# Performance work log

Measured on AMD Instinct MI355X. Metric: run time of the kernel, lower is better.

## Reference

```python
import jax, jax.numpy as jnp
import numpy as np

H = 4      # attention heads
C = 64     # hidden_dim per head
GAT_SLOPE = 0.2   # PyG GATConv leaky_relu negative_slope
ACT_SLOPE = 0.01  # nn.LeakyReLU / F.leaky_relu default


def gat_layer(x, src, dst, W, a_src, a_dst, b, n):
    # x: [n, F_in] -> h: [n, H, C]
    h = (x @ W).reshape(n, H, C)
    al_s = jnp.einsum('nhc,hc->nh', h, a_src)  # [n, H]
    al_d = jnp.einsum('nhc,hc->nh', h, a_dst)
    e = jax.nn.leaky_relu(al_s[src] + al_d[dst], GAT_SLOPE)  # [E, H]
    # segment softmax over destination nodes (self-loops ensure non-empty segments)
    m = jax.ops.segment_max(e, dst, num_segments=n)
    p = jnp.exp(e - m[dst])
    s = jax.ops.segment_sum(p, dst, num_segments=n)
    alpha = p / s[dst]
    out = jax.ops.segment_sum(h[src] * alpha[:, :, None], dst, num_segments=n)  # [n, H, C]
    return out.reshape(n, H * C) + b


def setup_inputs() -> dict:
    key = jax.random.key(0)
    ks = jax.random.split(key, 24)
    N, E = 102400, 409600
    F_IN, F_OUT = 80, 80
    HC = H * C
    RIN, RHID, ROUT = 60, 512, 60
    def g(k, shape, scale):
        return (jax.random.normal(k, shape, dtype=jnp.float32) * scale)
    inp = {
        'x': g(ks[0], (N, F_IN), 1.0),
        'edge_index': jax.random.randint(ks[1], (2, E), 0, N, dtype=jnp.int64),
        'root_ctx_norm': g(ks[2], (4096, RIN), 1.0),
        'W0': g(ks[3], (F_IN, HC), 0.1), 'a_src0': g(ks[4], (H, C), 0.1), 'a_dst0': g(ks[5], (H, C), 0.1), 'b0': jnp.zeros((HC,), jnp.float32),
        'W1': g(ks[6], (HC, HC), 0.06), 'a_src1': g(ks[7], (H, C), 0.1), 'a_dst1': g(ks[8], (H, C), 0.1), 'b1': jnp.zeros((HC,), jnp.float32),
        'W2': g(ks[9], (HC, HC), 0.06), 'a_src2': g(ks[10], (H, C), 0.1), 'a_dst2': g(ks[11], (H, C), 0.1), 'b2': jnp.zeros((HC,), jnp.float32),
        'fc_w': g(ks[12], (HC, F_OUT), 0.06), 'fc_b': jnp.zeros((F_OUT,), jnp.float32),
        'r_w1': g(ks[13], (RIN, RHID), 0.1), 'r_b1': jnp.zeros((RHID,), jnp.float32),
        'r_w2': g(ks[14], (RHID, RHID), 0.04), 'r_b2': jnp.zeros((RHID,), jnp.float32),
        'r_w3': g(ks[15], (RHID, ROUT), 0.04), 'r_b3': jnp.zeros((ROUT,), jnp.float32),
    }
    return inp


def reference(x, edge_index, root_ctx_norm,
              W0, a_src0, a_dst0, b0,
              W1, a_src1, a_dst1, b1,
              W2, a_src2, a_dst2, b2,
              fc_w, fc_b, r_w1, r_b1, r_w2, r_b2, r_w3, r_b3):
    n = x.shape[0]
    loops = jnp.arange(n, dtype=edge_index.dtype)
    src = jnp.concatenate([edge_index[0], loops])  # PyG add_self_loops=True
    dst = jnp.concatenate([edge_index[1], loops])
    h = gat_layer(x, src, dst, W0, a_src0, a_dst0, b0, n)
    h = jax.nn.leaky_relu(h, ACT_SLOPE)  # dropout is identity in eval
    h = gat_layer(h, src, dst, W1, a_src1, a_dst1, b1, n)
    h = jax.nn.leaky_relu(h, ACT_SLOPE)
    h = gat_layer(h, src, dst, W2, a_src2, a_dst2, b2, n)
    rot = h @ fc_w + fc_b
    r = jax.nn.leaky_relu(root_ctx_norm @ r_w1 + r_b1, ACT_SLOPE)
    r = jax.nn.leaky_relu(r @ r_w2 + r_b2, ACT_SLOPE)
    root_norm = r @ r_w3 + r_b3
    return rot, root_norm
```

## Files before the change

### kernel.cpp

```cpp
#include <hip/hip_runtime.h>
#include <hip/hip_bf16.h>


#define GAT_SLOPE 0.2f
#define ACT_SLOPE 0.01f

typedef unsigned short ushort_t;
typedef __attribute__((ext_vector_type(8))) short bf16x8;
typedef __attribute__((ext_vector_type(8))) unsigned short ushort8;
typedef __attribute__((ext_vector_type(4))) unsigned short ushort4v;
typedef __attribute__((ext_vector_type(4))) float floatx4;

__device__ __forceinline__ float lrelu(float x, float s) {
    return fmaxf(x, s * x);
}

__device__ __forceinline__ ushort_t f2bf(float f) {
    union { float f; unsigned u; } x; x.f = f;
    unsigned r = x.u + 0x7FFF + ((x.u >> 16) & 1);
    return (ushort_t)(r >> 16);
}

__device__ __forceinline__ float bf2f(ushort_t u) {
    union { unsigned u; float f; } x; x.u = ((unsigned)u) << 16;
    return x.f;
}

__global__ void detect_fmt(const int* __restrict__ raw, int nwords, int* flag) {
    __shared__ int nz;
    if (threadIdx.x == 0) nz = 0;
    __syncthreads();
    int lim = nwords < 4096 ? nwords : 4096;
    for (int i = threadIdx.x * 2 + 1; i < lim; i += 512)
        if (raw[i] != 0) atomicAdd(&nz, 1);
    __syncthreads();
    if (threadIdx.x == 0) *flag = (nz == 0) ? 1 : 0;
}

__global__ void zero2(int* __restrict__ a, int* __restrict__ b, int n) {
    int i = blockIdx.x * blockDim.x + threadIdx.x;
    if (i < n) { a[i] = 0; b[i] = 0; }
}

__global__ void convert_count(const int* __restrict__ raw, int E,
                              const int* __restrict__ flag,
                              int* __restrict__ idx32, int* __restrict__ counts) {
    int i = blockIdx.x * blockDim.x + threadIdx.x;
    if (i >= E) return;
    int f = *flag;
    int s = f ? raw[2 * i] : raw[i];
    int d = f ? raw[2 * (E + i)] : raw[E + i];
    idx32[i] = s;
    idx32[E + i] = d;
    atomicAdd(&counts[d], 1);
}

__global__ void scan_block(const int* __restrict__ counts, int* __restrict__ inc,
                           int* __restrict__ blockSums, int N) {
    __shared__ int sh[256];
    int i = blockIdx.x * 256 + threadIdx.x;
    int v = (i < N) ? counts[i] : 0;
    sh[threadIdx.x] = v;
    __syncthreads();
    for (int off = 1; off < 256; off <<= 1) {
        int t = (threadIdx.x >= off) ? sh[threadIdx.x - off] : 0;
        __syncthreads();
        sh[threadIdx.x] += t;
        __syncthreads();
    }
    if (i < N) inc[i] = sh[threadIdx.x];
    if (threadIdx.x == 255) blockSums[blockIdx.x] = sh[255];
}

__global__ void scan_sums(int* __restrict__ blockSums, int nb, int* __restrict__ row_ptr) {
    __shared__ int sh[512];
    int v = ((int)threadIdx.x < nb) ? blockSums[threadIdx.x] : 0;
    sh[threadIdx.x] = v;
    __syncthreads();
    for (int off = 1; off < 512; off <<= 1) {
        int t = (threadIdx.x >= off) ? sh[threadIdx.x - off] : 0;
        __syncthreads();
        sh[threadIdx.x] += t;
        __syncthreads();
    }
    if ((int)threadIdx.x < nb) blockSums[threadIdx.x] = sh[threadIdx.x];
    if (threadIdx.x == 0) row_ptr[0] = 0;
}

__global__ void scan_add(const int* __restrict__ inc, const int* __restrict__ blockSums,
                         int* __restrict__ row_ptr, int N) {
    int i = blockIdx.x * 256 + threadIdx.x;
    if (i < N) row_ptr[i + 1] = inc[i] + (blockIdx.x > 0 ? blockSums[blockIdx.x - 1] : 0);
}

__global__ void edge_fill(const int* __restrict__ src, const int* __restrict__ dst, int E,
                          const int* __restrict__ row_ptr, int* __restrict__ cursor,
                          int* __restrict__ col) {
    int i = blockIdx.x * blockDim.x + threadIdx.x;
    if (i < E) {
        int d = dst[i];
        int pos = row_ptr[d] + atomicAdd(&cursor[d], 1);
        col[pos] = src[i];
    }
}

__global__ void convert_bf4(const float* __restrict__ in, ushort_t* __restrict__ out, int n4) {
    int i = blockIdx.x * blockDim.x + threadIdx.x;
    if (i >= n4) return;
    const float4 v = ((const float4*)in)[i];
    ushort4v o;
    o.x = f2bf(v.x); o.y = f2bf(v.y); o.z = f2bf(v.z); o.w = f2bf(v.w);
    ((ushort4v*)out)[i] = o;
}

__global__ void convert_padrow(const float* __restrict__ in, ushort_t* __restrict__ out,
                               int M, int Kr, int Kp) {
    int i = blockIdx.x * blockDim.x + threadIdx.x;
    if (i >= M * Kp) return;
    int r = i / Kp, c = i - r * Kp;
    out[i] = f2bf((c < Kr) ? in[(size_t)r * Kr + c] : 0.f);
}

struct WConv { const float* in; ushort_t* out; int Kp, Kr, N, Npad, blkOff; };
struct WConvArr { WConv e[7]; int n; };

__global__ void convert_w_multi(WConvArr a) {
    int b = blockIdx.x;
    int ei = 0;
    for (int k = 1; k < a.n; k++)
        if (b >= a.e[k].blkOff) ei = k;
    WConv w = a.e[ei];
    int i = (b - w.blkOff) * 256 + threadIdx.x;
    if (i >= w.Npad * w.Kp) return;
    int n = i / w.Kp, k = i - n * w.Kp;
    float v = (n < w.N && k < w.Kr) ? w.in[(size_t)k * w.N + n] : 0.f;
    w.out[i] = f2bf(v);
}

#define LDA 40

__global__ __launch_bounds__(256) void gemm_mfma_gat(
    const ushort_t* __restrict__ A, const ushort_t* __restrict__ Bt,
    const float* __restrict__ a_src, const float* __restrict__ a_dst,
    ushort_t* __restrict__ Hbf, float* __restrict__ al_s, float* __restrict__ al_d,
    int M, int K) {
    const int NCOL = 256;
    __shared__ __align__(16) ushort_t As[128 * LDA];
    __shared__ __align__(16) ushort_t Bs[128 * LDA];
    int t = threadIdx.x;
    int wave = t >> 6, lane = t & 63;
    int wm = (wave >> 1) << 6;
    int wn = (wave & 1) << 6;
    int rowBase = blockIdx.y << 7;
    int colBase = blockIdx.x << 7;
    int lrow = lane & 15, lquad = lane >> 4;
    floatx4 acc[4][4];
#pragma unroll
    for (int i = 0; i < 4; i++)
#pragma unroll
        for (int j = 0; j < 4; j++) acc[i][j] = (floatx4){0.f, 0.f, 0.f, 0.f};

    int srow = t >> 2;
    int sko  = (t & 3) * 8;
    const ushort8 zero8 = {0, 0, 0, 0, 0, 0, 0, 0};

    for (int k0 = 0; k0 < K; k0 += 32) {
        bool kin = (k0 + sko + 8) <= K;
#pragma unroll
        for (int half = 0; half < 2; half++) {
            int row = srow + half * 64;
            ushort8 va = kin ? *(const ushort8*)(A + (size_t)(rowBase + row) * K + k0 + sko)
                             : zero8;
            *(ushort8*)(As + row * LDA + sko) = va;
            ushort8 vb = kin ? *(const ushort8*)(Bt + (size_t)(colBase + row) * K + k0 + sko)
                             : zero8;
            *(ushort8*)(Bs + row * LDA + sko) = vb;
        }
        __syncthreads();
        bf16x8 af[4], bfv[4];
#pragma unroll
        for (int i = 0; i < 4; i++)
            af[i] = *(const bf16x8*)(As + (wm + i * 16 + lrow) * LDA + lquad * 8);
#pragma unroll
        for (int j = 0; j < 4; j++)
            bfv[j] = *(const bf16x8*)(Bs + (wn + j * 16 + lrow) * LDA + lquad * 8);
#pragma unroll
        for (int i = 0; i < 4; i++)
#pragma unroll
            for (int j = 0; j < 4; j++)
                acc[i][j] = __builtin_amdgcn_mfma_f32_16x16x32_bf16(af[i], bfv[j],
                                                                    acc[i][j], 0, 0, 0);
        __syncthreads();
    }
    int head = (colBase + wn) >> 6;
    float avs[4], avd[4];
#pragma unroll
    for (int j = 0; j < 4; j++) {
        avs[j] = a_src[head * 64 + j * 16 + lrow];
        avd[j] = a_dst[head * 64 + j * 16 + lrow];
    }
#pragma unroll
    for (int i = 0; i < 4; i++) {
#pragma unroll
        for (int r = 0; r < 4; r++) {
            float ps = 0.f, pd = 0.f;
#pragma unroll
            for (int j = 0; j < 4; j++) {
                ps += acc[i][j][r] * avs[j];
                pd += acc[i][j][r] * avd[j];
            }
#pragma unroll
            for (int off = 1; off < 16; off <<= 1) {
                ps += __shfl_xor(ps, off);
                pd += __shfl_xor(pd, off);
            }
            if (lrow == 0) {
                int gr = rowBase + wm + i * 16 + lquad * 4 + r;
                al_s[gr * 4 + head] = ps;
                al_d[gr * 4 + head] = pd;
            }
        }
        int grb = rowBase + wm + i * 16 + lquad * 4;
#pragma unroll
        for (int j = 0; j < 4; j++) {
            int gc = colBase + wn + j * 16 + lrow;
#pragma unroll
            for (int r = 0; r < 4; r++)
                Hbf[(size_t)(grb + r) * NCOL + gc] = f2bf(acc[i][j][r]);
        }
    }
}

__global__ __launch_bounds__(256) void gemm_mfma(
    const ushort_t* __restrict__ A, const ushort_t* __restrict__ Bt,
    const float* __restrict__ bias, void* __restrict__ Cout,
    int M, int N, int K, int act, float slope, int outBf) {
    __shared__ __align__(16) ushort_t As[128 * LDA];
    __shared__ __align__(16) ushort_t Bs[128 * LDA];
    int t = threadIdx.x;
    int wave = t >> 6, lane = t & 63;
    int wm = (wave >> 1) << 6;
    int wn = (wave & 1) << 6;
    int rowBase = blockIdx.y << 7;
    int colBase = blockIdx.x << 7;
    int lrow = lane & 15, lquad = lane >> 4;
    floatx4 acc[4][4];
#pragma unroll
    for (int i = 0; i < 4; i++)
#pragma unroll
        for (int j = 0; j < 4; j++) acc[i][j] = (floatx4){0.f, 0.f, 0.f, 0.f};

    int srow = t >> 2;
    int sko  = (t & 3) * 8;
    const ushort8 zero8 = {0, 0, 0, 0, 0, 0, 0, 0};

    for (int k0 = 0; k0 < K; k0 += 32) {
        bool kin = (k0 + sko + 8) <= K;
#pragma unroll
        for (int half = 0; half < 2; half++) {
            int row = srow + half * 64;
            ushort8 va = kin ? *(const ushort8*)(A + (size_t)(rowBase + row) * K + k0 + sko)
                             : zero8;
            *(ushort8*)(As + row * LDA + sko) = va;
            ushort8 vb = kin ? *(const ushort8*)(Bt + (size_t)(colBase + row) * K + k0 + sko)
                             : zero8;
            *(ushort8*)(Bs + row * LDA + sko) = vb;
        }
        __syncthreads();
        bf16x8 af[4], bfv[4];
#pragma unroll
        for (int i = 0; i < 4; i++)
            af[i] = *(const bf16x8*)(As + (wm + i * 16 + lrow) * LDA + lquad * 8);
#pragma unroll
        for (int j = 0; j < 4; j++)
            bfv[j] = *(const bf16x8*)(Bs + (wn + j * 16 + lrow) * LDA + lquad * 8);
#pragma unroll
        for (int i = 0; i < 4; i++)
#pragma unroll
            for (int j = 0; j < 4; j++)
                acc[i][j] = __builtin_amdgcn_mfma_f32_16x16x32_bf16(af[i], bfv[j],
                                                                    acc[i][j], 0, 0, 0);
        __syncthreads();
    }
#pragma unroll
    for (int i = 0; i < 4; i++) {
        int gr = rowBase + wm + i * 16 + lquad * 4;
#pragma unroll
        for (int j = 0; j < 4; j++) {
            int gc = colBase + wn + j * 16 + lrow;
            if (gc >= N) continue;
            float b = bias ? bias[gc] : 0.f;
#pragma unroll
            for (int r = 0; r < 4; r++) {
                float v = acc[i][j][r] + b;
                if (act) v = lrelu(v, slope);
                if (outBf)
                    ((ushort_t*)Cout)[(size_t)(gr + r) * N + gc] = f2bf(v);
                else
                    ((float*)Cout)[(size_t)(gr + r) * N + gc] = v;
            }
        }
    }
}

__global__ __launch_bounds__(256) void gat_agg(
    const ushort_t* __restrict__ h_bf, const float* __restrict__ al_s,
    const float* __restrict__ al_d, const int* __restrict__ row_ptr,
    const int* __restrict__ col, const float* __restrict__ bias,
    ushort_t* __restrict__ out_bf, int N, int act, float slope) {
    int gw = __builtin_amdgcn_readfirstlane((blockIdx.x * 256 + threadIdx.x) >> 6);
    if (gw >= N) return;
    int lane = threadIdx.x & 63;
    int head = lane >> 4;
    int idx = gw * 4 + head;
    float ad = al_d[idx];
    const ushort4v* h4 = (const ushort4v*)h_bf;
    float p = __expf(lrelu(al_s[idx] + ad, GAT_SLOPE));
    ushort4v hv = h4[(size_t)gw * 64 + lane];
    float s = p;
    float4 acc;
    acc.x = p * bf2f(hv.x); acc.y = p * bf2f(hv.y);
    acc.z = p * bf2f(hv.z); acc.w = p * bf2f(hv.w);
    int beg = row_ptr[gw], end = row_ptr[gw + 1];
    for (int i = beg; i < end; i += 4) {
        int cnt = end - i;
        int sn0 = col[i];
        int sn1 = (cnt > 1) ? col[i + 1] : sn0;
        int sn2 = (cnt > 2) ? col[i + 2] : sn0;
        int sn3 = (cnt > 3) ? col[i + 3] : sn0;
        ushort4v h0 = h4[(size_t)sn0 * 64 + lane];
        ushort4v h1 = h4[(size_t)sn1 * 64 + lane];
        ushort4v h2 = h4[(size_t)sn2 * 64 + lane];
        ushort4v h3 = h4[(size_t)sn3 * 64 + lane];
        float a0 = al_s[sn0 * 4 + head];
        float a1 = al_s[sn1 * 4 + head];
        float a2 = al_s[sn2 * 4 + head];
        float a3 = al_s[sn3 * 4 + head];
        float p0 = __expf(lrelu(a0 + ad, GAT_SLOPE));
        acc.x += p0 * bf2f(h0.x); acc.y += p0 * bf2f(h0.y);
        acc.z += p0 * bf2f(h0.z); acc.w += p0 * bf2f(h0.w);
        s += p0;
        if (cnt > 1) {
            float p1 = __expf(lrelu(a1 + ad, GAT_SLOPE));
            acc.x += p1 * bf2f(h1.x); acc.y += p1 * bf2f(h1.y);
            acc.z += p1 * bf2f(h1.z); acc.w += p1 * bf2f(h1.w);
            s += p1;
        }
        if (cnt > 2) {
            float p2 = __expf(lrelu(a2 + ad, GAT_SLOPE));
            acc.x += p2 * bf2f(h2.x); acc.y += p2 * bf2f(h2.y);
            acc.z += p2 * bf2f(h2.z); acc.w += p2 * bf2f(h2.w);
            s += p2;
        }
        if (cnt > 3) {
            float p3 = __expf(lrelu(a3 + ad, GAT_SLOPE));
            acc.x += p3 * bf2f(h3.x); acc.y += p3 * bf2f(h3.y);
            acc.z += p3 * bf2f(h3.z); acc.w += p3 * bf2f(h3.w);
            s += p3;
        }
    }
    float rs = 1.f / s;
    float4 bv = ((const float4*)bias)[lane];
    acc.x = acc.x * rs + bv.x; acc.y = acc.y * rs + bv.y;
    acc.z = acc.z * rs + bv.z; acc.w = acc.w * rs + bv.w;
    if (act) {
        acc.x = lrelu(acc.x, slope); acc.y = lrelu(acc.y, slope);
        acc.z = lrelu(acc.z, slope); acc.w = lrelu(acc.w, slope);
    }
    ushort4v o;
    o.x = f2bf(acc.x); o.y = f2bf(acc.y); o.z = f2bf(acc.z); o.w = f2bf(acc.w);
    ((ushort4v*)out_bf)[(size_t)gw * 64 + lane] = o;
}

extern "C" void kernel_launch(void* const* d_in, const int* in_sizes, int n_in,
                              void* d_out, int out_size, void* d_ws, size_t ws_size,
                              hipStream_t stream) {
    const float* x        = (const float*)d_in[0];
    const int*   rawEdge  = (const int*)d_in[1];
    const float* rootCtx  = (const float*)d_in[2];
    const float* W[3]     = {(const float*)d_in[3], (const float*)d_in[7], (const float*)d_in[11]};
    const float* aS[3]    = {(const float*)d_in[4], (const float*)d_in[8], (const float*)d_in[12]};
    const float* aD[3]    = {(const float*)d_in[5], (const float*)d_in[9], (const float*)d_in[13]};
    const float* bb[3]    = {(const float*)d_in[6], (const float*)d_in[10], (const float*)d_in[14]};
    const float* fc_w     = (const float*)d_in[15];
    const float* fc_b     = (const float*)d_in[16];
    const float* r_w1     = (const float*)d_in[17];
    const float* r_b1     = (const float*)d_in[18];
    const float* r_w2     = (const float*)d_in[19];
    const float* r_b2     = (const float*)d_in[20];
    const float* r_w3     = (const float*)d_in[21];
    const float* r_b3     = (const float*)d_in[22];

    const int N  = in_sizes[0] / 80;
    const int E  = in_sizes[1] / 2;
    const int R  = in_sizes[2] / 60;
    const int N4 = N * 4;
    const int HC = 256;

    float* outRot  = (float*)d_out;
    float* outRoot = (float*)d_out + (size_t)N * 80;

    size_t off = 0;
    auto carve = [&](size_t bytes) -> void* {
        off = (off + 255) & ~(size_t)255;
        void* p = (char*)d_ws + off;
        off += bytes;
        return p;
    };
    int*      flag      = (int*)carve(4);
    int*      idx32     = (int*)carve((size_t)2 * E * 4);
    int*      counts    = (int*)carve((size_t)N * 4);
    int*      cursor    = (int*)carve((size_t)N * 4);
    int*      row_ptr   = (int*)carve((size_t)(N + 1) * 4);
    int*      incArr    = (int*)carve((size_t)N * 4);
    int*      blockSums = (int*)carve(512 * 4);
    int*      colArr    = (int*)carve((size_t)E * 4);
    float*    al_s      = (float*)carve((size_t)N4 * 4);
    float*    al_d      = (float*)carve((size_t)N4 * 4);
    ushort_t* h_bf      = (ushort_t*)carve((size_t)N * HC * 2);
    ushort_t* agg_bf    = (ushort_t*)carve((size_t)N * HC * 2);
    ushort_t* x_bf      = (ushort_t*)carve((size_t)N * 80 * 2);
    ushort_t* rc_bf     = (ushort_t*)carve((size_t)R * 64 * 2);
    ushort_t* t1_bf     = (ushort_t*)carve((size_t)R * 512 * 2);
    ushort_t* t2_bf     = (ushort_t*)carve((size_t)R * 512 * 2);
    ushort_t* Wt0       = (ushort_t*)carve((size_t)256 * 80 * 2);
    ushort_t* Wt1       = (ushort_t*)carve((size_t)256 * 256 * 2);
    ushort_t* Wt2       = (ushort_t*)carve((size_t)256 * 256 * 2);
    ushort_t* fcWt      = (ushort_t*)carve((size_t)128 * 256 * 2);
    ushort_t* rW1t      = (ushort_t*)carve((size_t)512 * 64 * 2);
    ushort_t* rWt2      = (ushort_t*)carve((size_t)512 * 512 * 2);
    ushort_t* rWt3      = (ushort_t*)carve((size_t)128 * 512 * 2);

    const int nb = (N + 255) / 256;
    dim3 blk(256);

    detect_fmt<<<1, 256, 0, stream>>>(rawEdge, 2 * E, flag);
    zero2<<<(N + 255) / 256, blk, 0, stream>>>(counts, cursor, N);
    convert_count<<<(E + 255) / 256, blk, 0, stream>>>(rawEdge, E, flag, idx32, counts);
    const int* srcArr = idx32;
    const int* dstArr = idx32 + E;
    scan_block<<<nb, 256, 0, stream>>>(counts, incArr, blockSums, N);
    scan_sums<<<1, 512, 0, stream>>>(blockSums, nb, row_ptr);
    scan_add<<<nb, 256, 0, stream>>>(incArr, blockSums, row_ptr, N);
    edge_fill<<<(E + 255) / 256, blk, 0, stream>>>(srcArr, dstArr, E, row_ptr, cursor, colArr);

    {
        WConvArr wa;
        auto mk = [&](int i, const float* in, ushort_t* out, int Kp, int Kr, int Nn, int Npad,
                      int blkOff) {
            wa.e[i] = WConv{in, out, Kp, Kr, Nn, Npad, blkOff};
        };
        int boff = 0;
        auto nblk = [](int Npad, int Kp) { return (Npad * Kp + 255) / 256; };
        mk(0, W[0], Wt0, 80, 80, 256, 256, boff);  boff += nblk(256, 80);
        mk(1, W[1], Wt1, 256, 256, 256, 256, boff); boff += nblk(256, 256);
        mk(2, W[2], Wt2, 256, 256, 256, 256, boff); boff += nblk(256, 256);
        mk(3, fc_w, fcWt, 256, 256, 80, 128, boff); boff += nblk(128, 256);
        mk(4, r_w1, rW1t, 64, 60, 512, 512, boff);  boff += nblk(512, 64);
        mk(5, r_w2, rWt2, 512, 512, 512, 512, boff); boff += nblk(512, 512);
        mk(6, r_w3, rWt3, 512, 512, 60, 128, boff);  boff += nblk(128, 512);
        wa.n = 7;
        convert_w_multi<<<boff, blk, 0, stream>>>(wa);
    }
    convert_bf4<<<(N * 80 / 4 + 255) / 256, blk, 0, stream>>>(x, x_bf, N * 80 / 4);
    convert_padrow<<<(R * 64 + 255) / 256, blk, 0, stream>>>(rootCtx, rc_bf, R, 60, 64);

    const ushort_t* curA = x_bf;
    int curK = 80;
    for (int l = 0; l < 3; l++) {
        dim3 g1(2, N / 128);
        gemm_mfma_gat<<<g1, blk, 0, stream>>>(curA, l == 0 ? Wt0 : (l == 1 ? Wt1 : Wt2),
                                              aS[l], aD[l], h_bf, al_s, al_d, N, curK);
        int act = (l < 2) ? 1 : 0;
        gat_agg<<<(N * 64 + 255) / 256, blk, 0, stream>>>(h_bf, al_s, al_d, row_ptr,
                                                          colArr, bb[l], agg_bf, N,
                                                          act, ACT_SLOPE);
        curA = agg_bf;
        curK = HC;
    }

    {
        dim3 g(1, N / 128);
        gemm_mfma<<<g, blk, 0, stream>>>(agg_bf, fcWt, fc_b, outRot, N, 80, HC, 0, 0.f, 0);
    }
    {
        dim3 g1(512 / 128, R / 128);
        gemm_mfma<<<g1, blk, 0, stream>>>(rc_bf, rW1t, r_b1, t1_bf, R, 512, 64,
                                          1, ACT_SLOPE, 1);
        dim3 g2(512 / 128, R / 128);
        gemm_mfma<<<g2, blk, 0, stream>>>(t1_bf, rWt2, r_b2, t2_bf, R, 512, 512,
                                          1, ACT_SLOPE, 1);
        dim3 g3(1, R / 128);
        gemm_mfma<<<g3, blk, 0, stream>>>(t2_bf, rWt3, r_b3, outRoot, R, 60, 512,
                                          0, 0.f, 0);
    }
}
```

Before: 542.8 us.

## Fuse GAT aggregation into next layer's MFMA GEMM via shared-memory A tile

Each layer's edge-softmax aggregation now runs as the prologue of the following GEMM. The 128-row aggregated tile is written straight into a swizzled 64KB LDS buffer and multiplied against weights read directly from global memory. The first layer converts x to bf16 inline, and the final fc GEMM is fused with layer-3 aggregation. This removes the agg_bf round trip and several launches. In exchange, occupancy drops because of the large LDS footprint, and the B operand is no longer staged through shared memory.

```diff
diff --git a/kernel.cpp b/kernel.cpp
--- a/kernel.cpp
+++ b/kernel.cpp
@@ -104,15 +104,6 @@
     }
 }
 
-__global__ void convert_bf4(const float* __restrict__ in, ushort_t* __restrict__ out, int n4) {
-    int i = blockIdx.x * blockDim.x + threadIdx.x;
-    if (i >= n4) return;
-    const float4 v = ((const float4*)in)[i];
-    ushort4v o;
-    o.x = f2bf(v.x); o.y = f2bf(v.y); o.z = f2bf(v.z); o.w = f2bf(v.w);
-    ((ushort4v*)out)[i] = o;
-}
-
 __global__ void convert_padrow(const float* __restrict__ in, ushort_t* __restrict__ out,
                                int M, int Kr, int Kp) {
     int i = blockIdx.x * blockDim.x + threadIdx.x;
@@ -137,22 +128,97 @@
     w.out[i] = f2bf(v);
 }
 
-#define LDA 40
-
-__global__ __launch_bounds__(256) void gemm_mfma_gat(
-    const ushort_t* __restrict__ A, const ushort_t* __restrict__ Bt,
+__global__ __launch_bounds__(512, 4) void fused_gat(
+    const float* __restrict__ xA,
+    const ushort_t* __restrict__ hPrev, const float* __restrict__ alsPrev,
+    const float* __restrict__ aldPrev, const int* __restrict__ row_ptr,
+    const int* __restrict__ col, const float* __restrict__ biasPrev, int actPrev,
+    const ushort_t* __restrict__ Bt, int strideB, int Kp, int strideA, int NpadB,
     const float* __restrict__ a_src, const float* __restrict__ a_dst,
     ushort_t* __restrict__ Hbf, float* __restrict__ al_s, float* __restrict__ al_d,
-    int M, int K) {
-    const int NCOL = 256;
-    __shared__ __align__(16) ushort_t As[128 * LDA];
-    __shared__ __align__(16) ushort_t Bs[128 * LDA];
+    float* __restrict__ Cout, const float* __restrict__ biasC, int Ncols) {
+    __shared__ ushort_t Af[128 * 256];
     int t = threadIdx.x;
     int wave = t >> 6, lane = t & 63;
-    int wm = (wave >> 1) << 6;
-    int wn = (wave & 1) << 6;
-    int rowBase = blockIdx.y << 7;
-    int colBase = blockIdx.x << 7;
+    int rowBase = blockIdx.x << 7;
+
+    if (xA) {
+        for (int idx = t; idx < 128 * Kp; idx += 512) {
+            int r = idx / Kp, c = idx - r * Kp;
+            float v = (c < 80) ? xA[(size_t)(rowBase + r) * 80 + c] : 0.f;
+            Af[r * strideA + (((c >> 3) ^ (r & 7)) << 3) + (c & 7)] = f2bf(v);
+        }
+    } else {
+        const ushort4v* h4 = (const ushort4v*)hPrev;
+        int head = lane >> 4;
+        float4 bv = ((const float4*)biasPrev)[lane];
+        for (int ii = 0; ii < 16; ii++) {
+            int nl = wave * 16 + ii;
+            int n = rowBase + nl;
+            int idx4 = n * 4 + head;
+            float ad = aldPrev[idx4];
+            float p = __expf(lrelu(alsPrev[idx4] + ad, GAT_SLOPE));
+            ushort4v hv = h4[(size_t)n * 64 + lane];
+            float s = p;
+            float4 acc;
+            acc.x = p * bf2f(hv.x); acc.y = p * bf2f(hv.y);
+            acc.z = p * bf2f(hv.z); acc.w = p * bf2f(hv.w);
+            int beg = row_ptr[n], end = row_ptr[n + 1];
+            for (int i = beg; i < end; i += 4) {
+                int cnt = end - i;
+                int sn0 = col[i];
+                int sn1 = (cnt > 1) ? col[i + 1] : sn0;
+                int sn2 = (cnt > 2) ? col[i + 2] : sn0;
+                int sn3 = (cnt > 3) ? col[i + 3] : sn0;
+                ushort4v h0 = h4[(size_t)sn0 * 64 + lane];
+                ushort4v h1 = h4[(size_t)sn1 * 64 + lane];
+                ushort4v h2 = h4[(size_t)sn2 * 64 + lane];
+                ushort4v h3 = h4[(size_t)sn3 * 64 + lane];
+                float a0 = alsPrev[sn0 * 4 + head];
+                float a1 = alsPrev[sn1 * 4 + head];
+                float a2 = alsPrev[sn2 * 4 + head];
+                float a3 = alsPrev[sn3 * 4 + head];
+                float p0 = __expf(lrelu(a0 + ad, GAT_SLOPE));
+                acc.x += p0 * bf2f(h0.x); acc.y += p0 * bf2f(h0.y);
+                acc.z += p0 * bf2f(h0.z); acc.w += p0 * bf2f(h0.w);
+                s += p0;
+                if (cnt > 1) {
+                    float p1 = __expf(lrelu(a1 + ad, GAT_SLOPE));
+                    acc.x += p1 * bf2f(h1.x); acc.y += p1 * bf2f(h1.y);
+                    acc.z += p1 * bf2f(h1.z); acc.w += p1 * bf2f(h1.w);
+                    s += p1;
+                }
+                if (cnt > 2) {
+                    float p2 = __expf(lrelu(a2 + ad, GAT_SLOPE));
+                    acc.x += p2 * bf2f(h2.x); acc.y += p2 * bf2f(h2.y);
+                    acc.z += p2 * bf2f(h2.z); acc.w += p2 * bf2f(h2.w);
+                    s += p2;
+                }
+                if (cnt > 3) {
+                    float p3 = __expf(lrelu(a3 + ad, GAT_SLOPE));
+                    acc.x += p3 * bf2f(h3.x); acc.y += p3 * bf2f(h3.y);
+                    acc.z += p3 * bf2f(h3.z); acc.w += p3 * bf2f(h3.w);
+                    s += p3;
+                }
+            }
+            float rs = 1.f / s;
+            acc.x = acc.x * rs + bv.x; acc.y = acc.y * rs + bv.y;
+            acc.z = acc.z * rs + bv.z; acc.w = acc.w * rs + bv.w;
+            if (actPrev) {
+                acc.x = lrelu(acc.x, ACT_SLOPE); acc.y = lrelu(acc.y, ACT_SLOPE);
+                acc.z = lrelu(acc.z, ACT_SLOPE); acc.w = lrelu(acc.w, ACT_SLOPE);
+            }
+            ushort4v o;
+            o.x = f2bf(acc.x); o.y = f2bf(acc.y); o.z = f2bf(acc.z); o.w = f2bf(acc.w);
+            *(ushort4v*)(Af + nl * strideA + (((lane >> 1) ^ (nl & 7)) << 3) +
+                         ((lane & 1) << 2)) = o;
+        }
+    }
+    __syncthreads();
+
+    int wm = (wave >> 2) << 6;
+    int wn = (wave & 3) << 6;
+    if (wn >= NpadB) return;
     int lrow = lane & 15, lquad = lane >> 4;
     floatx4 acc[4][4];
 #pragma unroll
@@ -160,77 +226,82 @@
 #pragma unroll
         for (int j = 0; j < 4; j++) acc[i][j] = (floatx4){0.f, 0.f, 0.f, 0.f};
 
-    int srow = t >> 2;
-    int sko  = (t & 3) * 8;
-    const ushort8 zero8 = {0, 0, 0, 0, 0, 0, 0, 0};
-
-    for (int k0 = 0; k0 < K; k0 += 32) {
-        bool kin = (k0 + sko + 8) <= K;
-#pragma unroll
-        for (int half = 0; half < 2; half++) {
-            int row = srow + half * 64;
-            ushort8 va = kin ? *(const ushort8*)(A + (size_t)(rowBase + row) * K + k0 + sko)
-                             : zero8;
-            *(ushort8*)(As + row * LDA + sko) = va;
-            ushort8 vb = kin ? *(const ushort8*)(Bt + (size_t)(colBase + row) * K + k0 + sko)
-                             : zero8;
-            *(ushort8*)(Bs + row * LDA + sko) = vb;
-        }
-        __syncthreads();
+    for (int k0 = 0; k0 < Kp; k0 += 32) {
+        int qbase = (k0 >> 3) + lquad;
         bf16x8 af[4], bfv[4];
 #pragma unroll
-        for (int i = 0; i < 4; i++)
-            af[i] = *(const bf16x8*)(As + (wm + i * 16 + lrow) * LDA + lquad * 8);
+        for (int i = 0; i < 4; i++) {
+            int r = wm + i * 16 + lrow;
+            af[i] = *(const bf16x8*)(Af + r * strideA + ((qbase ^ (r & 7)) << 3));
+        }
 #pragma unroll
         for (int j = 0; j < 4; j++)
-            bfv[j] = *(const bf16x8*)(Bs + (wn + j * 16 + lrow) * LDA + lquad * 8);
+            bfv[j] = *(const bf16x8*)(Bt + (size_t)(wn + j * 16 + lrow) * strideB +
+                                      k0 + lquad * 8);
 #pragma unroll
         for (int i = 0; i < 4; i++)
 #pragma unroll
             for (int j = 0; j < 4; j++)
                 acc[i][j] = __builtin_amdgcn_mfma_f32_16x16x32_bf16(af[i], bfv[j],
                                                                     acc[i][j], 0, 0, 0);
-        __syncthreads();
-    }
-    int head = (colBase + wn) >> 6;
-    float avs[4], avd[4];
-#pragma unroll
-    for (int j = 0; j < 4; j++) {
-        avs[j] = a_src[head * 64 + j * 16 + lrow];
-        avd[j] = a_dst[head * 64 + j * 16 + lrow];
-    }
-#pragma unroll
-    for (int i = 0; i < 4; i++) {
-#pragma unroll
-        for (int r = 0; r < 4; r++) {
-            float ps = 0.f, pd = 0.f;
+    }
+
+    if (a_src) {
+        int head = wn >> 6;
+        float avs[4], avd[4];
+#pragma unroll
+        for (int j = 0; j < 4; j++) {
+            avs[j] = a_src[head * 64 + j * 16 + lrow];
+            avd[j] = a_dst[head * 64 + j * 16 + lrow];
+        }
+#pragma unroll
+        for (int i = 0; i < 4; i++) {
+#pragma unroll
+            for (int r = 0; r < 4; r++) {
+                float ps = 0.f, pd = 0.f;
+#pragma unroll
+                for (int j = 0; j < 4; j++) {
+                    ps += acc[i][j][r] * avs[j];
+                    pd += acc[i][j][r] * avd[j];
+                }
+#pragma unroll
+                for (int off = 1; off < 16; off <<= 1) {
+                    ps += __shfl_xor(ps, off);
+                    pd += __shfl_xor(pd, off);
+                }
+                if (lrow == 0) {
+                    int gr = rowBase + wm + i * 16 + lquad * 4 + r;
+                    al_s[gr * 4 + head] = ps;
+                    al_d[gr * 4 + head] = pd;
+                }
+            }
+            int grb = rowBase + wm + i * 16 + lquad * 4;
 #pragma unroll
             for (int j = 0; j < 4; j++) {
-                ps += acc[i][j][r] * avs[j];
-                pd += acc[i][j][r] * avd[j];
-            }
-#pragma unroll
-            for (int off = 1; off < 16; off <<= 1) {
-                ps += __shfl_xor(ps, off);
-                pd += __shfl_xor(pd, off);
-            }
-            if (lrow == 0) {
-                int gr = rowBase + wm + i * 16 + lquad * 4 + r;
-                al_s[gr * 4 + head] = ps;
-                al_d[gr * 4 + head] = pd;
-            }
-        }
-        int grb = rowBase + wm + i * 16 + lquad * 4;
-#pragma unroll
-        for (int j = 0; j < 4; j++) {
-            int gc = colBase + wn + j * 16 + lrow;
-#pragma unroll
-            for (int r = 0; r < 4; r++)
-                Hbf[(size_t)(grb + r) * NCOL + gc] = f2bf(acc[i][j][r]);
-        }
-    }
-}
-
+                int gc = wn + j * 16 + lrow;
+#pragma unroll
+                for (int r = 0; r < 4; r++)
+                    Hbf[(size_t)(grb + r) * 256 + gc] = f2bf(acc[i][j][r]);
+            }
+        }
+    } else {
+#pragma unroll
+        for (int i = 0; i < 4; i++) {
+            int gr = rowBase + wm + i * 16 + lquad * 4;
+#pragma unroll
+            for (int j = 0; j < 4; j++) {
+                int gc = wn + j * 16 + lrow;
+                if (gc >= Ncols) continue;
+                float b = biasC[gc];
+#pragma unroll
+                for (int r = 0; r < 4; r++)
+                    Cout[(size_t)(gr + r) * Ncols + gc] = acc[i][j][r] + b;
+            }
+        }
+    }
+}
+
+#define LDA 40
 __global__ __launch_bounds__(256) void gemm_mfma(
     const ushort_t* __restrict__ A, const ushort_t* __restrict__ Bt,
     const float* __restrict__ bias, void* __restrict__ Cout,
@@ -301,75 +372,6 @@
             }
         }
     }
-}
-
-__global__ __launch_bounds__(256) void gat_agg(
-    const ushort_t* __restrict__ h_bf, const float* __restrict__ al_s,
-    const float* __restrict__ al_d, const int* __restrict__ row_ptr,
-    const int* __restrict__ col, const float* __restrict__ bias,
-    ushort_t* __restrict__ out_bf, int N, int act, float slope) {
-    int gw = __builtin_amdgcn_readfirstlane((blockIdx.x * 256 + threadIdx.x) >> 6);
-    if (gw >= N) return;
-    int lane = threadIdx.x & 63;
-    int head = lane >> 4;
-    int idx = gw * 4 + head;
-    float ad = al_d[idx];
-    const ushort4v* h4 = (const ushort4v*)h_bf;
-    float p = __expf(lrelu(al_s[idx] + ad, GAT_SLOPE));
-    ushort4v hv = h4[(size_t)gw * 64 + lane];
-    float s = p;
-    float4 acc;
-    acc.x = p * bf2f(hv.x); acc.y = p * bf2f(hv.y);
-    acc.z = p * bf2f(hv.z); acc.w = p * bf2f(hv.w);
-    int beg = row_ptr[gw], end = row_ptr[gw + 1];
-    for (int i = beg; i < end; i += 4) {
-        int cnt = end - i;
-        int sn0 = col[i];
-        int sn1 = (cnt > 1) ? col[i + 1] : sn0;
-        int sn2 = (cnt > 2) ? col[i + 2] : sn0;
-        int sn3 = (cnt > 3) ? col[i + 3] : sn0;
-        ushort4v h0 = h4[(size_t)sn0 * 64 + lane];
-        ushort4v h1 = h4[(size_t)sn1 * 64 + lane];
-        ushort4v h2 = h4[(size_t)sn2 * 64 + lane];
-        ushort4v h3 = h4[(size_t)sn3 * 64 + lane];
-        float a0 = al_s[sn0 * 4 + head];
-        float a1 = al_s[sn1 * 4 + head];
-        float a2 = al_s[sn2 * 4 + head];
-        float a3 = al_s[sn3 * 4 + head];
-        float p0 = __expf(lrelu(a0 + ad, GAT_SLOPE));
-        acc.x += p0 * bf2f(h0.x); acc.y += p0 * bf2f(h0.y);
-        acc.z += p0 * bf2f(h0.z); acc.w += p0 * bf2f(h0.w);
-        s += p0;
-        if (cnt > 1) {
-            float p1 = __expf(lrelu(a1 + ad, GAT_SLOPE));
-            acc.x += p1 * bf2f(h1.x); acc.y += p1 * bf2f(h1.y);
-            acc.z += p1 * bf2f(h1.z); acc.w += p1 * bf2f(h1.w);
-            s += p1;
-        }
-        if (cnt > 2) {
-            float p2 = __expf(lrelu(a2 + ad, GAT_SLOPE));
-            acc.x += p2 * bf2f(h2.x); acc.y += p2 * bf2f(h2.y);
-            acc.z += p2 * bf2f(h2.z); acc.w += p2 * bf2f(h2.w);
-            s += p2;
-        }
-        if (cnt > 3) {
-            float p3 = __expf(lrelu(a3 + ad, GAT_SLOPE));
-            acc.x += p3 * bf2f(h3.x); acc.y += p3 * bf2f(h3.y);
-            acc.z += p3 * bf2f(h3.z); acc.w += p3 * bf2f(h3.w);
-            s += p3;
-        }
-    }
-    float rs = 1.f / s;
-    float4 bv = ((const float4*)bias)[lane];
-    acc.x = acc.x * rs + bv.x; acc.y = acc.y * rs + bv.y;
-    acc.z = acc.z * rs + bv.z; acc.w = acc.w * rs + bv.w;
-    if (act) {
-        acc.x = lrelu(acc.x, slope); acc.y = lrelu(acc.y, slope);
-        acc.z = lrelu(acc.z, slope); acc.w = lrelu(acc.w, slope);
-    }
-    ushort4v o;
-    o.x = f2bf(acc.x); o.y = f2bf(acc.y); o.z = f2bf(acc.z); o.w = f2bf(acc.w);
-    ((ushort4v*)out_bf)[(size_t)gw * 64 + lane] = o;
 }
 
 extern "C" void kernel_launch(void* const* d_in, const int* in_sizes, int n_in,
@@ -395,7 +397,6 @@
     const int E  = in_sizes[1] / 2;
     const int R  = in_sizes[2] / 60;
     const int N4 = N * 4;
-    const int HC = 256;
 
     float* outRot  = (float*)d_out;
     float* outRoot = (float*)d_out + (size_t)N * 80;
@@ -415,15 +416,16 @@
     int*      incArr    = (int*)carve((size_t)N * 4);
     int*      blockSums = (int*)carve(512 * 4);
     int*      colArr    = (int*)carve((size_t)E * 4);
-    float*    al_s      = (float*)carve((size_t)N4 * 4);
-    float*    al_d      = (float*)carve((size_t)N4 * 4);
-    ushort_t* h_bf      = (ushort_t*)carve((size_t)N * HC * 2);
-    ushort_t* agg_bf    = (ushort_t*)carve((size_t)N * HC * 2);
-    ushort_t* x_bf      = (ushort_t*)carve((size_t)N * 80 * 2);
+    float*    alsA      = (float*)carve((size_t)N4 * 4);
+    float*    aldA      = (float*)carve((size_t)N4 * 4);
+    float*    alsB      = (float*)carve((size_t)N4 * 4);
+    float*    aldB      = (float*)carve((size_t)N4 * 4);
+    ushort_t* hA        = (ushort_t*)carve((size_t)N * 256 * 2);
+    ushort_t* hB        = (ushort_t*)carve((size_t)N * 256 * 2);
     ushort_t* rc_bf     = (ushort_t*)carve((size_t)R * 64 * 2);
     ushort_t* t1_bf     = (ushort_t*)carve((size_t)R * 512 * 2);
     ushort_t* t2_bf     = (ushort_t*)carve((size_t)R * 512 * 2);
-    ushort_t* Wt0       = (ushort_t*)carve((size_t)256 * 80 * 2);
+    ushort_t* Wt0       = (ushort_t*)carve((size_t)256 * 96 * 2);
     ushort_t* Wt1       = (ushort_t*)carve((size_t)256 * 256 * 2);
     ushort_t* Wt2       = (ushort_t*)carve((size_t)256 * 256 * 2);
     ushort_t* fcWt      = (ushort_t*)carve((size_t)128 * 256 * 2);
@@ -452,7 +454,7 @@
         };
         int boff = 0;
         auto nblk = [](int Npad, int Kp) { return (Npad * Kp + 255) / 256; };
-        mk(0, W[0], Wt0, 80, 80, 256, 256, boff);  boff += nblk(256, 80);
+        mk(0, W[0], Wt0, 96, 80, 256, 256, boff);   boff += nblk(256, 96);
         mk(1, W[1], Wt1, 256, 256, 256, 256, boff); boff += nblk(256, 256);
         mk(2, W[2], Wt2, 256, 256, 256, 256, boff); boff += nblk(256, 256);
         mk(3, fc_w, fcWt, 256, 256, 80, 128, boff); boff += nblk(128, 256);
@@ -462,27 +464,26 @@
         wa.n = 7;
         convert_w_multi<<<boff, blk, 0, stream>>>(wa);
     }
-    convert_bf4<<<(N * 80 / 4 + 255) / 256, blk, 0, stream>>>(x, x_bf, N * 80 / 4);
     convert_padrow<<<(R * 64 + 255) / 256, blk, 0, stream>>>(rootCtx, rc_bf, R, 60, 64);
 
-    const ushort_t* curA = x_bf;
-    int curK = 80;
-    for (int l = 0; l < 3; l++) {
-        dim3 g1(2, N / 128);
-        gemm_mfma_gat<<<g1, blk, 0, stream>>>(curA, l == 0 ? Wt0 : (l == 1 ? Wt1 : Wt2),
-                                              aS[l], aD[l], h_bf, al_s, al_d, N, curK);
-        int act = (l < 2) ? 1 : 0;
-        gat_agg<<<(N * 64 + 255) / 256, blk, 0, stream>>>(h_bf, al_s, al_d, row_ptr,
-                                                          colArr, bb[l], agg_bf, N,
-                                                          act, ACT_SLOPE);
-        curA = agg_bf;
-        curK = HC;
-    }
-
-    {
-        dim3 g(1, N / 128);
-        gemm_mfma<<<g, blk, 0, stream>>>(agg_bf, fcWt, fc_b, outRot, N, 80, HC, 0, 0.f, 0);
-    }
+    dim3 fgrid(N / 128);
+    dim3 fblk(512);
+    fused_gat<<<fgrid, fblk, 0, stream>>>(x, nullptr, nullptr, nullptr, nullptr, nullptr,
+                                          nullptr, 0, Wt0, 96, 96, 128, 256,
+                                          aS[0], aD[0], hA, alsA, aldA,
+                                          nullptr, nullptr, 0);
+    fused_gat<<<fgrid, fblk, 0, stream>>>(nullptr, hA, alsA, aldA, row_ptr, colArr,
+                                          bb[0], 1, Wt1, 256, 256, 256, 256,
+                                          aS[1], aD[1], hB, alsB, aldB,
+                                          nullptr, nullptr, 0);
+    fused_gat<<<fgrid, fblk, 0, stream>>>(nullptr, hB, alsB, aldB, row_ptr, colArr,
+                                          bb[1], 1, Wt2, 256, 256, 256, 256,
+                                          aS[2], aD[2], hA, alsA, aldA,
+                                          nullptr, nullptr, 0);
+    fused_gat<<<fgrid, fblk, 0, stream>>>(nullptr, hA, alsA, aldA, row_ptr, colArr,
+                                          bb[2], 0, fcWt, 256, 256, 256, 128,
+                                          nullptr, nullptr, nullptr, nullptr, nullptr,
+                                          outRot, fc_b, 80);
     {
         dim3 g1(512 / 128, R / 128);
         gemm_mfma<<<g1, blk, 0, stream>>>(rc_bf, rW1t, r_b1, t1_bf, R, 512, 64,
```

After: 612.2 us. 1.13x slower.

## Load GEMM fragments directly from global memory, dropping LDS staging and barriers

Applied to the files above, without the earlier changes.

Both MFMA GEMM kernels stop staging A and B tiles through shared memory with two barriers per K step. Each wave now loads its bf16x8 fragments straight from global memory. Because the K-bound check is gone, the layer-0 input and W0 are padded from K=80 to 96 so K is a multiple of 32. This removes LDS traffic and synchronisation, but each tile is now read by several waves through cache instead of once into LDS, and the padding adds bytes to convert x.

```diff
diff --git a/kernel.cpp b/kernel.cpp
--- a/kernel.cpp
+++ b/kernel.cpp
@@ -104,15 +104,6 @@
     }
 }
 
-__global__ void convert_bf4(const float* __restrict__ in, ushort_t* __restrict__ out, int n4) {
-    int i = blockIdx.x * blockDim.x + threadIdx.x;
-    if (i >= n4) return;
-    const float4 v = ((const float4*)in)[i];
-    ushort4v o;
-    o.x = f2bf(v.x); o.y = f2bf(v.y); o.z = f2bf(v.z); o.w = f2bf(v.w);
-    ((ushort4v*)out)[i] = o;
-}
-
 __global__ void convert_padrow(const float* __restrict__ in, ushort_t* __restrict__ out,
                                int M, int Kr, int Kp) {
     int i = blockIdx.x * blockDim.x + threadIdx.x;
@@ -137,16 +128,11 @@
     w.out[i] = f2bf(v);
 }
 
-#define LDA 40
-
-__global__ __launch_bounds__(256) void gemm_mfma_gat(
+__global__ __launch_bounds__(256) void gemm_gat(
     const ushort_t* __restrict__ A, const ushort_t* __restrict__ Bt,
     const float* __restrict__ a_src, const float* __restrict__ a_dst,
     ushort_t* __restrict__ Hbf, float* __restrict__ al_s, float* __restrict__ al_d,
     int M, int K) {
-    const int NCOL = 256;
-    __shared__ __align__(16) ushort_t As[128 * LDA];
-    __shared__ __align__(16) ushort_t Bs[128 * LDA];
     int t = threadIdx.x;
     int wave = t >> 6, lane = t & 63;
     int wm = (wave >> 1) << 6;
@@ -160,37 +146,27 @@
 #pragma unroll
         for (int j = 0; j < 4; j++) acc[i][j] = (floatx4){0.f, 0.f, 0.f, 0.f};
 
-    int srow = t >> 2;
-    int sko  = (t & 3) * 8;
-    const ushort8 zero8 = {0, 0, 0, 0, 0, 0, 0, 0};
+    const ushort_t* Ab[4];
+    const ushort_t* Bb[4];
+#pragma unroll
+    for (int i = 0; i < 4; i++)
+        Ab[i] = A + (size_t)(rowBase + wm + i * 16 + lrow) * K + lquad * 8;
+#pragma unroll
+    for (int j = 0; j < 4; j++)
+        Bb[j] = Bt + (size_t)(colBase + wn + j * 16 + lrow) * K + lquad * 8;
 
     for (int k0 = 0; k0 < K; k0 += 32) {
-        bool kin = (k0 + sko + 8) <= K;
-#pragma unroll
-        for (int half = 0; half < 2; half++) {
-            int row = srow + half * 64;
-            ushort8 va = kin ? *(const ushort8*)(A + (size_t)(rowBase + row) * K + k0 + sko)
-                             : zero8;
-            *(ushort8*)(As + row * LDA + sko) = va;
-            ushort8 vb = kin ? *(const ushort8*)(Bt + (size_t)(colBase + row) * K + k0 + sko)
-                             : zero8;
-            *(ushort8*)(Bs + row * LDA + sko) = vb;
-        }
-        __syncthreads();
         bf16x8 af[4], bfv[4];
 #pragma unroll
-        for (int i = 0; i < 4; i++)
-            af[i] = *(const bf16x8*)(As + (wm + i * 16 + lrow) * LDA + lquad * 8);
-#pragma unroll
-        for (int j = 0; j < 4; j++)
-            bfv[j] = *(const bf16x8*)(Bs + (wn + j * 16 + lrow) * LDA + lquad * 8);
+        for (int i = 0; i < 4; i++) af[i] = *(const bf16x8*)(Ab[i] + k0);
+#pragma unroll
+        for (int j = 0; j < 4; j++) bfv[j] = *(const bf16x8*)(Bb[j] + k0);
 #pragma unroll
         for (int i = 0; i < 4; i++)
 #pragma unroll
             for (int j = 0; j < 4; j++)
                 acc[i][j] = __builtin_amdgcn_mfma_f32_16x16x32_bf16(af[i], bfv[j],
                                                                     acc[i][j], 0, 0, 0);
-        __syncthreads();
     }
     int head = (colBase + wn) >> 6;
     float avs[4], avd[4];
@@ -226,17 +202,15 @@
             int gc = colBase + wn + j * 16 + lrow;
 #pragma unroll
             for (int r = 0; r < 4; r++)
-                Hbf[(size_t)(grb + r) * NCOL + gc] = f2bf(acc[i][j][r]);
-        }
-    }
-}
-
-__global__ __launch_bounds__(256) void gemm_mfma(
+                Hbf[(size_t)(grb + r) * 256 + gc] = f2bf(acc[i][j][r]);
+        }
+    }
+}
+
+__global__ __launch_bounds__(256) void gemm_plain(
     const ushort_t* __restrict__ A, const ushort_t* __restrict__ Bt,
     const float* __restrict__ bias, void* __restrict__ Cout,
     int M, int N, int K, int act, float slope, int outBf) {
-    __shared__ __align__(16) ushort_t As[128 * LDA];
-    __shared__ __align__(16) ushort_t Bs[128 * LDA];
     int t = threadIdx.x;
     int wave = t >> 6, lane = t & 63;
     int wm = (wave >> 1) << 6;
@@ -250,37 +224,27 @@
 #pragma unroll
         for (int j = 0; j < 4; j++) acc[i][j] = (floatx4){0.f, 0.f, 0.f, 0.f};
 
-    int srow = t >> 2;
-    int sko  = (t & 3) * 8;
-    const ushort8 zero8 = {0, 0, 0, 0, 0, 0, 0, 0};
+    const ushort_t* Ab[4];
+    const ushort_t* Bb[4];
+#pragma unroll
+    for (int i = 0; i < 4; i++)
+        Ab[i] = A + (size_t)(rowBase + wm + i * 16 + lrow) * K + lquad * 8;
+#pragma unroll
+    for (int j = 0; j < 4; j++)
+        Bb[j] = Bt + (size_t)(colBase + wn + j * 16 + lrow) * K + lquad * 8;
 
     for (int k0 = 0; k0 < K; k0 += 32) {
-        bool kin = (k0 + sko + 8) <= K;
-#pragma unroll
-        for (int half = 0; half < 2; half++) {
-            int row = srow + half * 64;
-            ushort8 va = kin ? *(const ushort8*)(A + (size_t)(rowBase + row) * K + k0 + sko)
-                             : zero8;
-            *(ushort8*)(As + row * LDA + sko) = va;
-            ushort8 vb = kin ? *(const ushort8*)(Bt + (size_t)(colBase + row) * K + k0 + sko)
-                             : zero8;
-            *(ushort8*)(Bs + row * LDA + sko) = vb;
-        }
-        __syncthreads();
         bf16x8 af[4], bfv[4];
 #pragma unroll
-        for (int i = 0; i < 4; i++)
-            af[i] = *(const bf16x8*)(As + (wm + i * 16 + lrow) * LDA + lquad * 8);
-#pragma unroll
-        for (int j = 0; j < 4; j++)
-            bfv[j] = *(const bf16x8*)(Bs + (wn + j * 16 + lrow) * LDA + lquad * 8);
+        for (int i = 0; i < 4; i++) af[i] = *(const bf16x8*)(Ab[i] + k0);
+#pragma unroll
+        for (int j = 0; j < 4; j++) bfv[j] = *(const bf16x8*)(Bb[j] + k0);
 #pragma unroll
         for (int i = 0; i < 4; i++)
 #pragma unroll
             for (int j = 0; j < 4; j++)
                 acc[i][j] = __builtin_amdgcn_mfma_f32_16x16x32_bf16(af[i], bfv[j],
                                                                     acc[i][j], 0, 0, 0);
-        __syncthreads();
     }
 #pragma unroll
     for (int i = 0; i < 4; i++) {
@@ -395,7 +359,6 @@
     const int E  = in_sizes[1] / 2;
     const int R  = in_sizes[2] / 60;
     const int N4 = N * 4;
-    const int HC = 256;
 
     float* outRot  = (float*)d_out;
     float* outRoot = (float*)d_out + (size_t)N * 80;
@@ -417,13 +380,13 @@
     int*      colArr    = (int*)carve((size_t)E * 4);
     float*    al_s      = (float*)carve((size_t)N4 * 4);
     float*    al_d      = (float*)carve((size_t)N4 * 4);
-    ushort_t* h_bf      = (ushort_t*)carve((size_t)N * HC * 2);
-    ushort_t* agg_bf    = (ushort_t*)carve((size_t)N * HC * 2);
-    ushort_t* x_bf      = (ushort_t*)carve((size_t)N * 80 * 2);
+    ushort_t* h_bf      = (ushort_t*)carve((size_t)N * 256 * 2);
+    ushort_t* agg_bf    = (ushort_t*)carve((size_t)N * 256 * 2);
+    ushort_t* x_bf      = (ushort_t*)carve((size_t)N * 96 * 2);
     ushort_t* rc_bf     = (ushort_t*)carve((size_t)R * 64 * 2);
     ushort_t* t1_bf     = (ushort_t*)carve((size_t)R * 512 * 2);
     ushort_t* t2_bf     = (ushort_t*)carve((size_t)R * 512 * 2);
-    ushort_t* Wt0       = (ushort_t*)carve((size_t)256 * 80 * 2);
+    ushort_t* Wt0       = (ushort_t*)carve((size_t)256 * 96 * 2);
     ushort_t* Wt1       = (ushort_t*)carve((size_t)256 * 256 * 2);
     ushort_t* Wt2       = (ushort_t*)carve((size_t)256 * 256 * 2);
     ushort_t* fcWt      = (ushort_t*)carve((size_t)128 * 256 * 2);
@@ -452,7 +415,7 @@
         };
         int boff = 0;
         auto nblk = [](int Npad, int Kp) { return (Npad * Kp + 255) / 256; };
-        mk(0, W[0], Wt0, 80, 80, 256, 256, boff);  boff += nblk(256, 80);
+        mk(0, W[0], Wt0, 96, 80, 256, 256, boff);   boff += nblk(256, 96);
         mk(1, W[1], Wt1, 256, 256, 256, 256, boff); boff += nblk(256, 256);
         mk(2, W[2], Wt2, 256, 256, 256, 256, boff); boff += nblk(256, 256);
         mk(3, fc_w, fcWt, 256, 256, 80, 128, boff); boff += nblk(128, 256);
@@ -462,36 +425,37 @@
         wa.n = 7;
         convert_w_multi<<<boff, blk, 0, stream>>>(wa);
     }
-    convert_bf4<<<(N * 80 / 4 + 255) / 256, blk, 0, stream>>>(x, x_bf, N * 80 / 4);
+    convert_padrow<<<(N * 96 + 255) / 256, blk, 0, stream>>>(x, x_bf, N, 80, 96);
     convert_padrow<<<(R * 64 + 255) / 256, blk, 0, stream>>>(rootCtx, rc_bf, R, 60, 64);
 
     const ushort_t* curA = x_bf;
-    int curK = 80;
+    int curK = 96;
     for (int l = 0; l < 3; l++) {
         dim3 g1(2, N / 128);
-        gemm_mfma_gat<<<g1, blk, 0, stream>>>(curA, l == 0 ? Wt0 : (l == 1 ? Wt1 : Wt2),
-                                              aS[l], aD[l], h_bf, al_s, al_d, N, curK);
+        gemm_gat<<<g1, blk, 0, stream>>>(curA, l == 0 ? Wt0 : (l == 1 ? Wt1 : Wt2),
+                                         aS[l], aD[l], h_bf, al_s, al_d, N, curK);
         int act = (l < 2) ? 1 : 0;
         gat_agg<<<(N * 64 + 255) / 256, blk, 0, stream>>>(h_bf, al_s, al_d, row_ptr,
                                                           colArr, bb[l], agg_bf, N,
                                                           act, ACT_SLOPE);
         curA = agg_bf;
-        curK = HC;
+        curK = 256;
     }
 
     {
         dim3 g(1, N / 128);
-        gemm_mfma<<<g, blk, 0, stream>>>(agg_bf, fcWt, fc_b, outRot, N, 80, HC, 0, 0.f, 0);
+        gemm_plain<<<g, blk, 0, stream>>>(agg_bf, fcWt, fc_b, outRot, N, 80, 256,
+                                          0, 0.f, 0);
     }
     {
         dim3 g1(512 / 128, R / 128);
-        gemm_mfma<<<g1, blk, 0, stream>>>(rc_bf, rW1t, r_b1, t1_bf, R, 512, 64,
-                                          1, ACT_SLOPE, 1);
+        gemm_plain<<<g1, blk, 0, stream>>>(rc_bf, rW1t, r_b1, t1_bf, R, 512, 64,
+                                           1, ACT_SLOPE, 1);
         dim3 g2(512 / 128, R / 128);
-        gemm_mfma<<<g2, blk, 0, stream>>>(t1_bf, rWt2, r_b2, t2_bf, R, 512, 512,
-                                          1, ACT_SLOPE, 1);
+        gemm_plain<<<g2, blk, 0, stream>>>(t1_bf, rWt2, r_b2, t2_bf, R, 512, 512,
+                                           1, ACT_SLOPE, 1);
         dim3 g3(1, R / 128);
-        gemm_mfma<<<g3, blk, 0, stream>>>(t2_bf, rWt3, r_b3, outRoot, R, 60, 512,
-                                          0, 0.f, 0);
-    }
-}
+        gemm_plain<<<g3, blk, 0, stream>>>(t2_bf, rWt3, r_b3, outRoot, R, 60, 512,
+                                           0, 0.f, 0);
+    }
+}
```

After: 603.6 us. 11.2% more time.
